# Optimization experiments

Measured on AMD Instinct MI355X. Metric: run time of the kernel, lower is better.

The kernel has to match this reference:

```python
import jax, jax.numpy as jnp
import numpy as np

N_NODES = 100000
N_EDGES = 1600000
FEAT = 128
LAYERS = [128, 128, 64]


def setup_inputs() -> dict:
    key = jax.random.key(0)
    ks = jax.random.split(key, 10)
    x = jax.random.normal(ks[0], (N_NODES, FEAT), dtype=jnp.float32)
    edge_index = jax.random.randint(ks[1], (2, N_EDGES), 0, N_NODES, dtype=jnp.int32)
    edge_weight = jax.random.uniform(ks[2], (N_EDGES,), dtype=jnp.float32)
    # GCNConv params (glorot weights + zero bias)
    def glorot(k, fi, fo):
        s = jnp.sqrt(6.0 / (fi + fo)).astype(jnp.float32)
        return jax.random.uniform(k, (fi, fo), jnp.float32, -s, s)
    W1 = glorot(ks[3], FEAT, LAYERS[0]); b1 = jnp.zeros((LAYERS[0],), jnp.float32)
    W2 = glorot(ks[4], LAYERS[0], LAYERS[1]); b2 = jnp.zeros((LAYERS[1],), jnp.float32)
    W3 = glorot(ks[5], LAYERS[1], LAYERS[2]); b3 = jnp.zeros((LAYERS[2],), jnp.float32)
    return {"x": x, "edge_index": edge_index, "edge_weight": edge_weight,
            "W1": W1, "b1": b1, "W2": W2, "b2": b2, "W3": W3, "b3": b3}


def _gcn_norm(edge_index, edge_weight, n_nodes):
    # symmetric normalization, no self loops (add_self_loops=False)
    src, dst = edge_index[0], edge_index[1]
    deg = jax.ops.segment_sum(edge_weight, dst, num_segments=n_nodes)
    dinv = jnp.where(deg > 0, jax.lax.rsqrt(jnp.maximum(deg, 1e-30)), 0.0)
    return dinv[src] * edge_weight * dinv[dst]


def _gcn_conv(h, src, dst, norm, W, b, n_nodes):
    h = h @ W                                  # linear first (PyG GCNConv)
    msg = norm[:, None] * h[src]               # [E, out_dim] gather
    out = jax.ops.segment_sum(msg, dst, num_segments=n_nodes)
    return out + b


def reference(x, edge_index, edge_weight, W1, b1, W2, b2, W3, b3):
    n = x.shape[0]
    src, dst = edge_index[0], edge_index[1]
    norm = _gcn_norm(edge_index, edge_weight, n)
    h = _gcn_conv(x, src, dst, norm, W1, b1, n)
    h = jax.nn.relu(h)                          # dropout = identity (eval)
    h = _gcn_conv(h, src, dst, norm, W2, b2, n)
    h = jax.nn.relu(h)
    h = _gcn_conv(h, src, dst, norm, W3, b3, n)
    return (h, h)
```

## Files before the change

### kernel.cpp

```cpp
#include <hip/hip_runtime.h>
#include <hip/hip_bf16.h>
#include <stdint.h>

#define N_NODES 100000
#define N_EDGES 1600000
#define SCAN_NB 98

typedef __bf16 bf16x8 __attribute__((ext_vector_type(8)));
typedef float f32x4 __attribute__((ext_vector_type(4)));
typedef unsigned short u16;

__device__ __forceinline__ u16 f2b(float f) {
    uint32_t u = __builtin_bit_cast(uint32_t, f);
    uint32_t r = (u + 0x7fffu + ((u >> 16) & 1u)) >> 16;
    return (u16)r;
}
__device__ __forceinline__ float b2f(uint32_t lo16) {
    return __builtin_bit_cast(float, lo16 << 16);
}

__global__ void rank_kernel(const int* __restrict__ dstp, int* __restrict__ cnt,
                            u16* __restrict__ rank) {
    int e = blockIdx.x * 256 + threadIdx.x;
    if (e >= N_EDGES) return;
    rank[e] = (u16)atomicAdd(&cnt[dstp[e]], 1);
}

__global__ __launch_bounds__(1024) void scan1(const int* __restrict__ cnt,
                                              int* __restrict__ rowptr,
                                              int* __restrict__ bsum) {
    __shared__ int ws[16];
    int t = threadIdx.x;
    int i = blockIdx.x * 1024 + t;
    int lane = t & 63, wid = t >> 6;
    int v = (i < N_NODES) ? cnt[i] : 0;
    int x = v;
    #pragma unroll
    for (int off = 1; off < 64; off <<= 1) {
        int y = __shfl_up(x, off, 64);
        if (lane >= off) x += y;
    }
    if (lane == 63) ws[wid] = x;
    __syncthreads();
    int woff = 0;
    for (int j = 0; j < wid; j++) woff += ws[j];
    if (i < N_NODES) rowptr[i] = woff + x - v;
    if (t == 1023) bsum[blockIdx.x] = woff + x;
}

__global__ void scan2(const int* __restrict__ bsum, int* __restrict__ boff,
                      int* __restrict__ rowptr) {
    int lane = threadIdx.x;
    int carry = 0;
    for (int base = 0; base < SCAN_NB; base += 64) {
        int b = base + lane;
        int v = (b < SCAN_NB) ? bsum[b] : 0;
        int x = v;
        #pragma unroll
        for (int off = 1; off < 64; off <<= 1) {
            int y = __shfl_up(x, off, 64);
            if (lane >= off) x += y;
        }
        if (b < SCAN_NB) boff[b] = carry + x - v;
        carry += __shfl(x, 63, 64);
    }
    if (lane == 0) rowptr[N_NODES] = carry;
}

__global__ __launch_bounds__(1024) void scan3(int* __restrict__ rowptr,
                                              const int* __restrict__ boff) {
    int i = blockIdx.x * 1024 + threadIdx.x;
    if (i < N_NODES) rowptr[i] += boff[blockIdx.x];
}

__global__ void scatter_kernel(const int* __restrict__ srcp, const int* __restrict__ dstp,
                               const float* __restrict__ w, const int* __restrict__ rowptr,
                               const u16* __restrict__ rank, int2* __restrict__ csr) {
    int e = blockIdx.x * 256 + threadIdx.x;
    if (e >= N_EDGES) return;
    int pos = rowptr[dstp[e]] + (int)rank[e];
    int2 m;
    m.x = srcp[e];
    m.y = __float_as_int(w[e]);
    csr[pos] = m;
}

__global__ __launch_bounds__(256) void deg_kernel(const int2* __restrict__ csr,
                                                  const int* __restrict__ rowptr,
                                                  float* __restrict__ dinv) {
    int node = (blockIdx.x * 256 + threadIdx.x) >> 6;
    if (node >= N_NODES) return;
    int lane = threadIdx.x & 63;
    int jb = rowptr[node], je = rowptr[node + 1];
    float s = 0.f;
    for (int j = jb + lane; j < je; j += 64) s += __int_as_float(csr[j].y);
    #pragma unroll
    for (int off = 32; off; off >>= 1) s += __shfl_down(s, off, 64);
    if (lane == 0) dinv[node] = (s > 0.f) ? rsqrtf(fmaxf(s, 1e-30f)) : 0.f;
}

__global__ void wconv_all(const float* __restrict__ W1, const float* __restrict__ W2,
                          const float* __restrict__ W3, u16* __restrict__ Wt1,
                          u16* __restrict__ Wt2, u16* __restrict__ Wt3) {
    int i = blockIdx.x * 256 + threadIdx.x;
    if (i < 16384) {
        int k = i >> 7, n = i & 127;
        Wt1[n * 128 + k] = f2b(W1[i]);
    } else if (i < 32768) {
        int j = i - 16384;
        int k = j >> 7, n = j & 127;
        Wt2[n * 128 + k] = f2b(W2[j]);
    } else if (i < 40960) {
        int j = i - 32768;
        int k = j >> 6, n = j & 63;
        Wt3[n * 128 + k] = f2b(W3[j]);
    }
}

__global__ __launch_bounds__(256) void gemm_f32A(const float* __restrict__ A,
                                                 const u16* __restrict__ Bt,
                                                 const float* __restrict__ dinv,
                                                 u16* __restrict__ C, int Dout) {
    int wid = (blockIdx.x * 256 + threadIdx.x) >> 6;
    if (wid >= N_NODES / 16) return;
    int lane = threadIdx.x & 63;
    int m = lane & 15;
    int k0 = (lane >> 4) * 8;
    int r0 = wid * 16;
    const float* ap = A + (size_t)(r0 + m) * 128 + k0;
    bf16x8 a[4];
    #pragma unroll
    for (int q = 0; q < 4; q++) {
        float4 lo = *(const float4*)(ap + q * 32);
        float4 hi = *(const float4*)(ap + q * 32 + 4);
        union { u16 s[8]; bf16x8 v; } u_;
        u_.s[0] = f2b(lo.x); u_.s[1] = f2b(lo.y); u_.s[2] = f2b(lo.z); u_.s[3] = f2b(lo.w);
        u_.s[4] = f2b(hi.x); u_.s[5] = f2b(hi.y); u_.s[6] = f2b(hi.z); u_.s[7] = f2b(hi.w);
        a[q] = u_.v;
    }
    int ntiles = Dout >> 4;
    int rbase = r0 + ((lane >> 4) << 2);
    float dv[4];
    #pragma unroll
    for (int i2 = 0; i2 < 4; i2++) dv[i2] = dinv[rbase + i2];
    for (int tn = 0; tn < ntiles; tn++) {
        const u16* bp = Bt + (size_t)(tn * 16 + m) * 128 + k0;
        f32x4 acc = {0.f, 0.f, 0.f, 0.f};
        acc = __builtin_amdgcn_mfma_f32_16x16x32_bf16(a[0], *(const bf16x8*)(bp + 0),  acc, 0, 0, 0);
        acc = __builtin_amdgcn_mfma_f32_16x16x32_bf16(a[1], *(const bf16x8*)(bp + 32), acc, 0, 0, 0);
        acc = __builtin_amdgcn_mfma_f32_16x16x32_bf16(a[2], *(const bf16x8*)(bp + 64), acc, 0, 0, 0);
        acc = __builtin_amdgcn_mfma_f32_16x16x32_bf16(a[3], *(const bf16x8*)(bp + 96), acc, 0, 0, 0);
        int col = tn * 16 + m;
        #pragma unroll
        for (int i2 = 0; i2 < 4; i2++)
            C[(size_t)(rbase + i2) * Dout + col] = f2b(acc[i2] * dv[i2]);
    }
}

__global__ __launch_bounds__(256) void gemm_bf16(const u16* __restrict__ A,
                                                 const u16* __restrict__ Bt,
                                                 const float* __restrict__ dinv,
                                                 u16* __restrict__ C, int Dout) {
    int wid = (blockIdx.x * 256 + threadIdx.x) >> 6;
    if (wid >= N_NODES / 16) return;
    int lane = threadIdx.x & 63;
    int m = lane & 15;
    int k0 = (lane >> 4) * 8;
    int r0 = wid * 16;
    const u16* ap = A + (size_t)(r0 + m) * 128 + k0;
    bf16x8 a0 = *(const bf16x8*)(ap + 0);
    bf16x8 a1 = *(const bf16x8*)(ap + 32);
    bf16x8 a2 = *(const bf16x8*)(ap + 64);
    bf16x8 a3 = *(const bf16x8*)(ap + 96);
    int ntiles = Dout >> 4;
    int rbase = r0 + ((lane >> 4) << 2);
    float dv[4];
    #pragma unroll
    for (int i2 = 0; i2 < 4; i2++) dv[i2] = dinv[rbase + i2];
    for (int tn = 0; tn < ntiles; tn++) {
        const u16* bp = Bt + (size_t)(tn * 16 + m) * 128 + k0;
        f32x4 acc = {0.f, 0.f, 0.f, 0.f};
        acc = __builtin_amdgcn_mfma_f32_16x16x32_bf16(a0, *(const bf16x8*)(bp + 0),  acc, 0, 0, 0);
        acc = __builtin_amdgcn_mfma_f32_16x16x32_bf16(a1, *(const bf16x8*)(bp + 32), acc, 0, 0, 0);
        acc = __builtin_amdgcn_mfma_f32_16x16x32_bf16(a2, *(const bf16x8*)(bp + 64), acc, 0, 0, 0);
        acc = __builtin_amdgcn_mfma_f32_16x16x32_bf16(a3, *(const bf16x8*)(bp + 96), acc, 0, 0, 0);
        int col = tn * 16 + m;
        #pragma unroll
        for (int i2 = 0; i2 < 4; i2++)
            C[(size_t)(rbase + i2) * Dout + col] = f2b(acc[i2] * dv[i2]);
    }
}

__global__ __launch_bounds__(256) void agg128(const u16* __restrict__ H,
                                              const int* __restrict__ row_ptr,
                                              const int2* __restrict__ csr,
                                              const float* __restrict__ dinv,
                                              const float* __restrict__ bias,
                                              u16* __restrict__ out, int do_relu) {
    int node = (blockIdx.x * 256 + threadIdx.x) >> 6;
    if (node >= N_NODES) return;
    int lane = threadIdx.x & 63;
    int c = lane * 2;
    float a0 = 0.f, a1 = 0.f;
    int jb = row_ptr[node], je = row_ptr[node + 1];
    for (int base = jb; base < je; base += 64) {
        int n = je - base;
        if (n > 64) n = 64;
        int2 meta;
        if (base + lane < je) meta = csr[base + lane];
        else { meta.x = 0; meta.y = 0; }
        for (int e = 0; e < n; e += 8) {
            int s[8]; float w[8];
            #pragma unroll
            for (int u = 0; u < 8; u++) {
                int idx = e + u;
                int sv = __shfl(meta.x, idx, 64);
                int wv = __shfl(meta.y, idx, 64);
                bool ok = idx < n;
                s[u] = ok ? sv : 0;
                w[u] = ok ? __int_as_float(wv) : 0.f;
            }
            uint32_t p[8];
            #pragma unroll
            for (int u = 0; u < 8; u++)
                p[u] = *(const uint32_t*)(H + (size_t)s[u] * 128 + c);
            #pragma unroll
            for (int u = 0; u < 8; u++) {
                a0 += w[u] * b2f(p[u] & 0xffffu);
                a1 += w[u] * b2f(p[u] >> 16);
            }
        }
    }
    float dv = dinv[node];
    a0 = dv * a0 + bias[c];
    a1 = dv * a1 + bias[c + 1];
    if (do_relu) { a0 = fmaxf(a0, 0.f); a1 = fmaxf(a1, 0.f); }
    uint32_t o = (uint32_t)f2b(a0) | ((uint32_t)f2b(a1) << 16);
    *(uint32_t*)(out + (size_t)node * 128 + c) = o;
}

__global__ __launch_bounds__(256) void agg64_out(const u16* __restrict__ H,
                                                 const int* __restrict__ row_ptr,
                                                 const int2* __restrict__ csr,
                                                 const float* __restrict__ dinv,
                                                 const float* __restrict__ bias,
                                                 float* __restrict__ out) {
    int wv = (blockIdx.x * 256 + threadIdx.x) >> 6;
    int node = wv * 2 + ((threadIdx.x >> 5) & 1);
    if (node >= N_NODES) return;
    int lane = threadIdx.x & 31;
    int c = lane * 2;
    float a0 = 0.f, a1 = 0.f;
    int jb = row_ptr[node], je = row_ptr[node + 1];
    for (int base = jb; base < je; base += 32) {
        int n = je - base;
        if (n > 32) n = 32;
        int2 meta;
        if (base + lane < je) meta = csr[base + lane];
        else { meta.x = 0; meta.y = 0; }
        for (int e = 0; e < n; e += 8) {
            int s[8]; float w[8];
            #pragma unroll
            for (int u = 0; u < 8; u++) {
                int idx = e + u;
                int sv = __shfl(meta.x, idx, 32);
                int wv2 = __shfl(meta.y, idx, 32);
                bool ok = idx < n;
                s[u] = ok ? sv : 0;
                w[u] = ok ? __int_as_float(wv2) : 0.f;
            }
            uint32_t p[8];
            #pragma unroll
            for (int u = 0; u < 8; u++)
                p[u] = *(const uint32_t*)(H + (size_t)s[u] * 64 + c);
            #pragma unroll
            for (int u = 0; u < 8; u++) {
                a0 += w[u] * b2f(p[u] & 0xffffu);
                a1 += w[u] * b2f(p[u] >> 16);
            }
        }
    }
    float dv = dinv[node];
    a0 = dv * a0 + bias[c];
    a1 = dv * a1 + bias[c + 1];
    size_t o = (size_t)node * 64 + c;
    float2 r; r.x = a0; r.y = a1;
    *(float2*)(out + o) = r;
    *(float2*)(out + (size_t)N_NODES * 64 + o) = r;
}

extern "C" void kernel_launch(void* const* d_in, const int* in_sizes, int n_in,
                              void* d_out, int out_size, void* d_ws, size_t ws_size,
                              hipStream_t stream) {
    const float* x  = (const float*)d_in[0];
    const int* eidx = (const int*)d_in[1];
    const float* ew = (const float*)d_in[2];
    const float* W1 = (const float*)d_in[3];
    const float* b1 = (const float*)d_in[4];
    const float* W2 = (const float*)d_in[5];
    const float* b2 = (const float*)d_in[6];
    const float* W3 = (const float*)d_in[7];
    const float* b3 = (const float*)d_in[8];
    const int* srcp = eidx;
    const int* dstp = eidx + N_EDGES;

    char* ws = (char*)d_ws;
    size_t off = 0;
    auto alloc = [&](size_t bytes) -> void* {
        void* p = ws + off;
        off += (bytes + 255) & ~(size_t)255;
        return p;
    };
    int*   cnt    = (int*)  alloc((size_t)N_NODES * 4);
    int*   rowptr = (int*)  alloc((size_t)(N_NODES + 1) * 4);
    int*   bsum   = (int*)  alloc(SCAN_NB * 4);
    int*   boff   = (int*)  alloc(SCAN_NB * 4);
    u16*   rank   = (u16*)  alloc((size_t)N_EDGES * 2);
    int2*  csr    = (int2*) alloc((size_t)N_EDGES * 8);
    float* dinv   = (float*)alloc((size_t)N_NODES * 4);
    u16*   Wt1    = (u16*)  alloc(128 * 128 * 2);
    u16*   Wt2    = (u16*)  alloc(128 * 128 * 2);
    u16*   Wt3    = (u16*)  alloc(128 * 64 * 2);
    u16*   bufA   = (u16*)  alloc((size_t)N_NODES * 128 * 2);
    u16*   bufB   = (u16*)  alloc((size_t)N_NODES * 128 * 2);

    hipMemsetAsync(cnt, 0, (size_t)N_NODES * 4, stream);

    rank_kernel<<<N_EDGES / 256, 256, 0, stream>>>(dstp, cnt, rank);
    scan1<<<SCAN_NB, 1024, 0, stream>>>(cnt, rowptr, bsum);
    scan2<<<1, 64, 0, stream>>>(bsum, boff, rowptr);
    scan3<<<SCAN_NB, 1024, 0, stream>>>(rowptr, boff);
    scatter_kernel<<<N_EDGES / 256, 256, 0, stream>>>(srcp, dstp, ew, rowptr, rank, csr);
    deg_kernel<<<N_NODES / 4, 256, 0, stream>>>(csr, rowptr, dinv);
    wconv_all<<<160, 256, 0, stream>>>(W1, W2, W3, Wt1, Wt2, Wt3);

    int gemm_blocks = (N_NODES / 16 + 3) / 4;
    gemm_f32A<<<gemm_blocks, 256, 0, stream>>>(x, Wt1, dinv, bufA, 128);
    agg128<<<N_NODES / 4, 256, 0, stream>>>(bufA, rowptr, csr, dinv, b1, bufB, 1);
    gemm_bf16<<<gemm_blocks, 256, 0, stream>>>(bufB, Wt2, dinv, bufA, 128);
    agg128<<<N_NODES / 4, 256, 0, stream>>>(bufA, rowptr, csr, dinv, b2, bufB, 1);
    gemm_bf16<<<gemm_blocks, 256, 0, stream>>>(bufB, Wt3, dinv, bufA, 64);
    agg64_out<<<N_NODES / 8, 256, 0, stream>>>(bufA, rowptr, csr, dinv, b3, (float*)d_out);
}
```

Before: 468.2 us.

## Build CSR via two-level bucketed radix partition instead of global atomics

Replaces the per-edge global-atomic rank, three-pass node scan, and random-address scatter with a two-level partition. Edges are first bucketed by dst>>8 using shared-memory histograms and a partitioned scatter into a temporary buffer that reuses bufA. A per-bucket kernel then builds rowptr, degree/dinv and the final CSR entirely with LDS atomics. This aims to cut global atomic contention and scattered writes, at the cost of an extra 16-byte-per-edge pass and non-deterministic edge order within rows.

```diff
diff --git a/kernel.cpp b/kernel.cpp
--- a/kernel.cpp
+++ b/kernel.cpp
@@ -4,7 +4,9 @@
 
 #define N_NODES 100000
 #define N_EDGES 1600000
-#define SCAN_NB 98
+#define NB_P 400
+#define EPP 4000
+#define NBUCK 391
 
 typedef __bf16 bf16x8 __attribute__((ext_vector_type(8)));
 typedef float f32x4 __attribute__((ext_vector_type(4)));
@@ -19,84 +21,139 @@
     return __builtin_bit_cast(float, lo16 << 16);
 }
 
-__global__ void rank_kernel(const int* __restrict__ dstp, int* __restrict__ cnt,
-                            u16* __restrict__ rank) {
-    int e = blockIdx.x * 256 + threadIdx.x;
-    if (e >= N_EDGES) return;
-    rank[e] = (u16)atomicAdd(&cnt[dstp[e]], 1);
-}
-
-__global__ __launch_bounds__(1024) void scan1(const int* __restrict__ cnt,
-                                              int* __restrict__ rowptr,
-                                              int* __restrict__ bsum) {
-    __shared__ int ws[16];
-    int t = threadIdx.x;
-    int i = blockIdx.x * 1024 + t;
-    int lane = t & 63, wid = t >> 6;
-    int v = (i < N_NODES) ? cnt[i] : 0;
-    int x = v;
+__global__ __launch_bounds__(256) void part_hist(const int* __restrict__ dstp,
+                                                 int* __restrict__ hist) {
+    __shared__ int h[NBUCK];
+    int t = threadIdx.x, p = blockIdx.x;
+    for (int b = t; b < NBUCK; b += 256) h[b] = 0;
+    __syncthreads();
+    int e0 = p * EPP;
+    for (int i = t; i < EPP; i += 256)
+        atomicAdd(&h[dstp[e0 + i] >> 8], 1);
+    __syncthreads();
+    for (int b = t; b < NBUCK; b += 256) hist[b * NB_P + p] = h[b];
+}
+
+__global__ void bucket_totals(const int* __restrict__ hist, int* __restrict__ totals) {
+    int w = (blockIdx.x * 256 + threadIdx.x) >> 6;
+    if (w >= NBUCK) return;
+    int lane = threadIdx.x & 63;
+    int s = 0;
+    for (int p = lane; p < NB_P; p += 64) s += hist[w * NB_P + p];
     #pragma unroll
-    for (int off = 1; off < 64; off <<= 1) {
-        int y = __shfl_up(x, off, 64);
-        if (lane >= off) x += y;
-    }
-    if (lane == 63) ws[wid] = x;
-    __syncthreads();
-    int woff = 0;
-    for (int j = 0; j < wid; j++) woff += ws[j];
-    if (i < N_NODES) rowptr[i] = woff + x - v;
-    if (t == 1023) bsum[blockIdx.x] = woff + x;
-}
-
-__global__ void scan2(const int* __restrict__ bsum, int* __restrict__ boff,
-                      int* __restrict__ rowptr) {
+    for (int off = 32; off; off >>= 1) s += __shfl_down(s, off, 64);
+    if (lane == 0) totals[w] = s;
+}
+
+__global__ void bucket_scan(const int* __restrict__ totals, int* __restrict__ base,
+                            int* __restrict__ rowptr) {
     int lane = threadIdx.x;
     int carry = 0;
-    for (int base = 0; base < SCAN_NB; base += 64) {
-        int b = base + lane;
-        int v = (b < SCAN_NB) ? bsum[b] : 0;
+    for (int s0 = 0; s0 < NBUCK; s0 += 64) {
+        int b = s0 + lane;
+        int v = (b < NBUCK) ? totals[b] : 0;
         int x = v;
         #pragma unroll
         for (int off = 1; off < 64; off <<= 1) {
             int y = __shfl_up(x, off, 64);
             if (lane >= off) x += y;
         }
-        if (b < SCAN_NB) boff[b] = carry + x - v;
+        if (b < NBUCK) base[b] = carry + x - v;
         carry += __shfl(x, 63, 64);
     }
-    if (lane == 0) rowptr[N_NODES] = carry;
-}
-
-__global__ __launch_bounds__(1024) void scan3(int* __restrict__ rowptr,
-                                              const int* __restrict__ boff) {
-    int i = blockIdx.x * 1024 + threadIdx.x;
-    if (i < N_NODES) rowptr[i] += boff[blockIdx.x];
-}
-
-__global__ void scatter_kernel(const int* __restrict__ srcp, const int* __restrict__ dstp,
-                               const float* __restrict__ w, const int* __restrict__ rowptr,
-                               const u16* __restrict__ rank, int2* __restrict__ csr) {
-    int e = blockIdx.x * 256 + threadIdx.x;
-    if (e >= N_EDGES) return;
-    int pos = rowptr[dstp[e]] + (int)rank[e];
-    int2 m;
-    m.x = srcp[e];
-    m.y = __float_as_int(w[e]);
-    csr[pos] = m;
-}
-
-__global__ __launch_bounds__(256) void deg_kernel(const int2* __restrict__ csr,
-                                                  const int* __restrict__ rowptr,
-                                                  float* __restrict__ dinv) {
-    int node = (blockIdx.x * 256 + threadIdx.x) >> 6;
-    if (node >= N_NODES) return;
+    if (lane == 0) { base[NBUCK] = carry; rowptr[N_NODES] = carry; }
+}
+
+__global__ void bucket_off(const int* __restrict__ hist, const int* __restrict__ base,
+                           int* __restrict__ off) {
+    int w = (blockIdx.x * 256 + threadIdx.x) >> 6;
+    if (w >= NBUCK) return;
     int lane = threadIdx.x & 63;
-    int jb = rowptr[node], je = rowptr[node + 1];
-    float s = 0.f;
-    for (int j = jb + lane; j < je; j += 64) s += __int_as_float(csr[j].y);
+    int run = base[w];
+    for (int s0 = 0; s0 < NB_P; s0 += 64) {
+        int p = s0 + lane;
+        int v = (p < NB_P) ? hist[w * NB_P + p] : 0;
+        int x = v;
+        #pragma unroll
+        for (int o = 1; o < 64; o <<= 1) {
+            int y = __shfl_up(x, o, 64);
+            if (lane >= o) x += y;
+        }
+        if (p < NB_P) off[w * NB_P + p] = run + x - v;
+        run += __shfl(x, 63, 64);
+    }
+}
+
+__global__ __launch_bounds__(256) void part_scatter(const int* __restrict__ srcp,
+                                                    const int* __restrict__ dstp,
+                                                    const float* __restrict__ ew,
+                                                    const int* __restrict__ off,
+                                                    int4* __restrict__ part) {
+    __shared__ int cur[NBUCK];
+    int t = threadIdx.x, p = blockIdx.x;
+    for (int b = t; b < NBUCK; b += 256) cur[b] = off[b * NB_P + p];
+    __syncthreads();
+    int e0 = p * EPP;
+    for (int i = t; i < EPP; i += 256) {
+        int e = e0 + i;
+        int s = srcp[e], d = dstp[e];
+        float w = ew[e];
+        int pos = atomicAdd(&cur[d >> 8], 1);
+        int4 E;
+        E.x = s; E.y = d; E.z = __float_as_int(w); E.w = 0;
+        part[pos] = E;
+    }
+}
+
+__global__ __launch_bounds__(256) void bucket_build(const int4* __restrict__ part,
+                                                    const int* __restrict__ base,
+                                                    int* __restrict__ rowptr,
+                                                    float* __restrict__ dinv,
+                                                    int2* __restrict__ csr) {
+    __shared__ int h[256];
+    __shared__ float dw[256];
+    __shared__ int cur[256];
+    __shared__ int wsum[4];
+    int t = threadIdx.x, b = blockIdx.x;
+    h[t] = 0; dw[t] = 0.f;
+    __syncthreads();
+    int jb = base[b], je = base[b + 1];
+    for (int i = jb + t; i < je; i += 256) {
+        int4 E = part[i];
+        int li = E.y & 255;
+        atomicAdd(&h[li], 1);
+        atomicAdd(&dw[li], __int_as_float(E.z));
+    }
+    __syncthreads();
+    int lane = t & 63, wid = t >> 6;
+    int v = h[t];
+    int x = v;
     #pragma unroll
-    for (int off = 32; off; off >>= 1) s += __shfl_down(s, off, 64);
-    if (lane == 0) dinv[node] = (s > 0.f) ? rsqrtf(fmaxf(s, 1e-30f)) : 0.f;
+    for (int o = 1; o < 64; o <<= 1) {
+        int y = __shfl_up(x, o, 64);
+        if (lane >= o) x += y;
+    }
+    if (lane == 63) wsum[wid] = x;
+    __syncthreads();
+    int woff = 0;
+    for (int j = 0; j < wid; j++) woff += wsum[j];
+    int excl = jb + woff + x - v;
+    int node = b * 256 + t;
+    if (node < N_NODES) {
+        rowptr[node] = excl;
+        float s = dw[t];
+        dinv[node] = (s > 0.f) ? rsqrtf(fmaxf(s, 1e-30f)) : 0.f;
+    }
+    cur[t] = excl;
+    __syncthreads();
+    for (int i = jb + t; i < je; i += 256) {
+        int4 E = part[i];
+        int li = E.y & 255;
+        int pos = atomicAdd(&cur[li], 1);
+        int2 c;
+        c.x = E.x; c.y = E.z;
+        csr[pos] = c;
+    }
 }
 
 __global__ void wconv_all(const float* __restrict__ W1, const float* __restrict__ W2,
@@ -305,17 +362,17 @@
     const int* dstp = eidx + N_EDGES;
 
     char* ws = (char*)d_ws;
-    size_t off = 0;
+    size_t off_ = 0;
     auto alloc = [&](size_t bytes) -> void* {
-        void* p = ws + off;
-        off += (bytes + 255) & ~(size_t)255;
+        void* p = ws + off_;
+        off_ += (bytes + 255) & ~(size_t)255;
         return p;
     };
-    int*   cnt    = (int*)  alloc((size_t)N_NODES * 4);
+    int*   hist   = (int*)  alloc((size_t)NBUCK * NB_P * 4);
+    int*   offm   = (int*)  alloc((size_t)NBUCK * NB_P * 4);
+    int*   totals = (int*)  alloc((size_t)NBUCK * 4);
+    int*   base   = (int*)  alloc((size_t)(NBUCK + 1) * 4);
     int*   rowptr = (int*)  alloc((size_t)(N_NODES + 1) * 4);
-    int*   bsum   = (int*)  alloc(SCAN_NB * 4);
-    int*   boff   = (int*)  alloc(SCAN_NB * 4);
-    u16*   rank   = (u16*)  alloc((size_t)N_EDGES * 2);
     int2*  csr    = (int2*) alloc((size_t)N_EDGES * 8);
     float* dinv   = (float*)alloc((size_t)N_NODES * 4);
     u16*   Wt1    = (u16*)  alloc(128 * 128 * 2);
@@ -323,15 +380,14 @@
     u16*   Wt3    = (u16*)  alloc(128 * 64 * 2);
     u16*   bufA   = (u16*)  alloc((size_t)N_NODES * 128 * 2);
     u16*   bufB   = (u16*)  alloc((size_t)N_NODES * 128 * 2);
-
-    hipMemsetAsync(cnt, 0, (size_t)N_NODES * 4, stream);
-
-    rank_kernel<<<N_EDGES / 256, 256, 0, stream>>>(dstp, cnt, rank);
-    scan1<<<SCAN_NB, 1024, 0, stream>>>(cnt, rowptr, bsum);
-    scan2<<<1, 64, 0, stream>>>(bsum, boff, rowptr);
-    scan3<<<SCAN_NB, 1024, 0, stream>>>(rowptr, boff);
-    scatter_kernel<<<N_EDGES / 256, 256, 0, stream>>>(srcp, dstp, ew, rowptr, rank, csr);
-    deg_kernel<<<N_NODES / 4, 256, 0, stream>>>(csr, rowptr, dinv);
+    int4*  part   = (int4*)bufA;
+
+    part_hist<<<NB_P, 256, 0, stream>>>(dstp, hist);
+    bucket_totals<<<(NBUCK + 3) / 4, 256, 0, stream>>>(hist, totals);
+    bucket_scan<<<1, 64, 0, stream>>>(totals, base, rowptr);
+    bucket_off<<<(NBUCK + 3) / 4, 256, 0, stream>>>(hist, base, offm);
+    part_scatter<<<NB_P, 256, 0, stream>>>(srcp, dstp, ew, offm, part);
+    bucket_build<<<NBUCK, 256, 0, stream>>>(part, base, rowptr, dinv, csr);
     wconv_all<<<160, 256, 0, stream>>>(W1, W2, W3, Wt1, Wt2, Wt3);
 
     int gemm_blocks = (N_NODES / 16 + 3) / 4;
```

New measurement: 422.3 us. -9.8%, faster.
